# Performance work log

Measured on AMD Instinct MI355X. Metric: run time of the kernel, lower is better.

## Reference

```python
import jax, jax.numpy as jnp
import numpy as np


def _maxpool(x, k):
    # non-overlapping kxk max pool (kernel == stride), NCHW
    B, C, H, W = x.shape
    return x.reshape(B, C, H // k, k, W // k, k).max(axis=(3, 5))


def setup_inputs() -> dict:
    key = jax.random.key(0)
    k1, k2, k3, k4 = jax.random.split(key, 4)
    return {
        "x1": jax.random.normal(k1, (8, 128, 128, 128), dtype=jnp.float32),
        "x2": jax.random.normal(k2, (8, 32, 256, 256), dtype=jnp.float32),
        "x3": jax.random.normal(k3, (8, 2, 512, 512), dtype=jnp.float32),
        "pure_ff": jax.random.normal(k4, (8, 256, 64, 64), dtype=jnp.float32),
    }


def reference(x1, x2, x3, pure_ff):
    # torch.cat([x,x],1) repeated n times duplicates the whole channel block
    # 2^n times; pooling duplicated channels equals pooling once then tiling.
    y1 = jnp.tile(_maxpool(x1, 2), (1, 2, 1, 1))    # 1 cat  -> x2 channels
    y2 = jnp.tile(_maxpool(x2, 4), (1, 8, 1, 1))    # 3 cats -> x8 channels
    y3 = jnp.tile(_maxpool(x3, 8), (1, 128, 1, 1))  # 7 cats -> x128 channels
    return jax.nn.relu(y1 + y2 + y3 + pure_ff)
```

## Files before the change

kernel.cpp:

```cpp
#include <hip/hip_runtime.h>
#include <math.h>


__global__ __launch_bounds__(256) void fused_ff_block3(
    const float* __restrict__ x1, const float* __restrict__ x2,
    const float* __restrict__ x3, const float* __restrict__ ff,
    float* __restrict__ out)
{
    __shared__ float y2s[32][64];
    __shared__ float y3s[2][64];

    const int bid = blockIdx.x;
    const int b   = bid >> 6;
    const int h   = bid & 63;
    const int tid = threadIdx.x;

    if (tid < 128) {
        const int c3 = tid >> 6;
        const int w  = tid & 63;
        const float* p = x3 + (size_t)b * 524288 + (size_t)c3 * 262144
                            + (size_t)(h * 8) * 512 + (size_t)w * 8;
        float m = -INFINITY;
        #pragma unroll
        for (int r = 0; r < 8; ++r) {
            const float4 a = *reinterpret_cast<const float4*>(p + (size_t)r * 512);
            const float4 c = *reinterpret_cast<const float4*>(p + (size_t)r * 512 + 4);
            m = fmaxf(m, fmaxf(fmaxf(fmaxf(a.x, a.y), fmaxf(a.z, a.w)),
                               fmaxf(fmaxf(c.x, c.y), fmaxf(c.z, c.w))));
        }
        y3s[c3][w] = m;
    }

    #pragma unroll
    for (int v = tid; v < 2048; v += 256) {
        const int c2 = v >> 6;
        const int w  = v & 63;
        const float* p = x2 + (size_t)b * 2097152 + (size_t)c2 * 65536
                            + (size_t)(h * 4) * 256 + (size_t)w * 4;
        float m = -INFINITY;
        #pragma unroll
        for (int r = 0; r < 4; ++r) {
            const float4 a = *reinterpret_cast<const float4*>(p + (size_t)r * 256);
            m = fmaxf(m, fmaxf(fmaxf(a.x, a.y), fmaxf(a.z, a.w)));
        }
        y2s[c2][w] = m;
    }

    __syncthreads();

    const int w     = tid & 63;
    const int clane = tid >> 6;
    #pragma unroll 4
    for (int it = 0; it < 32; ++it) {
        const int c1 = it * 4 + clane;
        const float* p = x1 + (size_t)b * 2097152 + (size_t)c1 * 16384
                            + (size_t)(h * 2) * 128 + (size_t)w * 2;
        const float2 a  = *reinterpret_cast<const float2*>(p);
        const float2 bb = *reinterpret_cast<const float2*>(p + 128);
        const float p1 = fmaxf(fmaxf(a.x, a.y), fmaxf(bb.x, bb.y));
        const float s  = p1 + y2s[c1 & 31][w] + y3s[c1 & 1][w];

        const size_t obase = (size_t)b * 1048576 + (size_t)h * 64 + (size_t)w;
        const size_t o0 = obase + (size_t)c1 * 4096;
        const size_t o1 = obase + (size_t)(c1 + 128) * 4096;
        out[o0] = fmaxf(s + ff[o0], 0.0f);
        out[o1] = fmaxf(s + ff[o1], 0.0f);
    }
}

extern "C" void kernel_launch(void* const* d_in, const int* in_sizes, int n_in,
                              void* d_out, int out_size, void* d_ws, size_t ws_size,
                              hipStream_t stream) {
    const float* x1 = (const float*)d_in[0];
    const float* x2 = (const float*)d_in[1];
    const float* x3 = (const float*)d_in[2];
    const float* ff = (const float*)d_in[3];
    float* out = (float*)d_out;

    dim3 grid(512);
    dim3 block(256);
    fused_ff_block3<<<grid, block, 0, stream>>>(x1, x2, x3, ff, out);
}
```

Measured before the change: 37.06 us.

## Split rows into width quarters, vectorize loads/stores, shuffle-reduce x3 pooling

```diff
diff --git a/kernel.cpp b/kernel.cpp
--- a/kernel.cpp
+++ b/kernel.cpp
@@ -2,69 +2,101 @@
 #include <math.h>
 
 
-__global__ __launch_bounds__(256) void fused_ff_block3(
+__global__ __launch_bounds__(256, 8) void fused_ff_block3(
     const float* __restrict__ x1, const float* __restrict__ x2,
     const float* __restrict__ x3, const float* __restrict__ ff,
     float* __restrict__ out)
 {
-    __shared__ float y2s[32][64];
-    __shared__ float y3s[2][64];
+    __shared__ float y2s[32][16];
+    __shared__ float y3s[2][16];
 
     const int bid = blockIdx.x;
-    const int b   = bid >> 6;
-    const int h   = bid & 63;
+    const int wq  = bid & 3;
+    const int h   = (bid >> 2) & 63;
+    const int b   = bid >> 8;
     const int tid = threadIdx.x;
 
-    if (tid < 128) {
-        const int c3 = tid >> 6;
-        const int w  = tid & 63;
-        const float* p = x3 + (size_t)b * 524288 + (size_t)c3 * 262144
-                            + (size_t)(h * 8) * 512 + (size_t)w * 8;
-        float m = -INFINITY;
-        #pragma unroll
-        for (int r = 0; r < 8; ++r) {
-            const float4 a = *reinterpret_cast<const float4*>(p + (size_t)r * 512);
-            const float4 c = *reinterpret_cast<const float4*>(p + (size_t)r * 512 + 4);
-            m = fmaxf(m, fmaxf(fmaxf(fmaxf(a.x, a.y), fmaxf(a.z, a.w)),
-                               fmaxf(fmaxf(c.x, c.y), fmaxf(c.z, c.w))));
-        }
-        y3s[c3][w] = m;
+    const int lane = tid & 63;
+    const int o3   = (tid >> 6) * 8 + (lane >> 3);
+    const int r3   = lane & 7;
+    const int c3   = o3 >> 4;
+    const int w3   = o3 & 15;
+    const float* p3 = x3 + (size_t)b * 524288 + (size_t)c3 * 262144
+                    + (size_t)(h * 8 + r3) * 512 + (size_t)(wq * 16 + w3) * 8;
+    const float4 a3 = *reinterpret_cast<const float4*>(p3);
+    const float4 b3 = *reinterpret_cast<const float4*>(p3 + 4);
+
+    #pragma unroll
+    for (int it = 0; it < 2; ++it) {
+        const int v  = tid + it * 256;
+        const int c2 = v >> 4;
+        const int w2 = v & 15;
+        const float* p = x2 + (size_t)b * 2097152 + (size_t)c2 * 65536
+                       + (size_t)(h * 4) * 256 + (size_t)(wq * 16 + w2) * 4;
+        const float4 q0 = *reinterpret_cast<const float4*>(p);
+        const float4 q1 = *reinterpret_cast<const float4*>(p + 256);
+        const float4 q2 = *reinterpret_cast<const float4*>(p + 512);
+        const float4 q3 = *reinterpret_cast<const float4*>(p + 768);
+        float m = fmaxf(fmaxf(fmaxf(q0.x, q0.y), fmaxf(q0.z, q0.w)),
+                        fmaxf(fmaxf(q1.x, q1.y), fmaxf(q1.z, q1.w)));
+        m = fmaxf(m, fmaxf(fmaxf(q2.x, q2.y), fmaxf(q2.z, q2.w)));
+        m = fmaxf(m, fmaxf(fmaxf(q3.x, q3.y), fmaxf(q3.z, q3.w)));
+        y2s[c2][w2] = m;
     }
 
-    #pragma unroll
-    for (int v = tid; v < 2048; v += 256) {
-        const int c2 = v >> 6;
-        const int w  = v & 63;
-        const float* p = x2 + (size_t)b * 2097152 + (size_t)c2 * 65536
-                            + (size_t)(h * 4) * 256 + (size_t)w * 4;
-        float m = -INFINITY;
-        #pragma unroll
-        for (int r = 0; r < 4; ++r) {
-            const float4 a = *reinterpret_cast<const float4*>(p + (size_t)r * 256);
-            m = fmaxf(m, fmaxf(fmaxf(a.x, a.y), fmaxf(a.z, a.w)));
-        }
-        y2s[c2][w] = m;
-    }
+    float m3 = fmaxf(fmaxf(fmaxf(a3.x, a3.y), fmaxf(a3.z, a3.w)),
+                     fmaxf(fmaxf(b3.x, b3.y), fmaxf(b3.z, b3.w)));
+    m3 = fmaxf(m3, __shfl_xor(m3, 1, 64));
+    m3 = fmaxf(m3, __shfl_xor(m3, 2, 64));
+    m3 = fmaxf(m3, __shfl_xor(m3, 4, 64));
+    if (r3 == 0) y3s[c3][w3] = m3;
 
     __syncthreads();
 
-    const int w     = tid & 63;
-    const int clane = tid >> 6;
-    #pragma unroll 4
-    for (int it = 0; it < 32; ++it) {
-        const int c1 = it * 4 + clane;
+    const int w4  = tid & 3;
+    const int c1b = tid >> 2;
+    #pragma unroll
+    for (int it = 0; it < 2; ++it) {
+        const int c1 = c1b + it * 64;
         const float* p = x1 + (size_t)b * 2097152 + (size_t)c1 * 16384
-                            + (size_t)(h * 2) * 128 + (size_t)w * 2;
-        const float2 a  = *reinterpret_cast<const float2*>(p);
-        const float2 bb = *reinterpret_cast<const float2*>(p + 128);
-        const float p1 = fmaxf(fmaxf(a.x, a.y), fmaxf(bb.x, bb.y));
-        const float s  = p1 + y2s[c1 & 31][w] + y3s[c1 & 1][w];
+                       + (size_t)(h * 2) * 128 + (size_t)(wq * 16 + w4 * 4) * 2;
+        const float4 a0 = *reinterpret_cast<const float4*>(p);
+        const float4 a1 = *reinterpret_cast<const float4*>(p + 4);
+        const float4 r0 = *reinterpret_cast<const float4*>(p + 128);
+        const float4 r1 = *reinterpret_cast<const float4*>(p + 132);
+        float4 y1v;
+        y1v.x = fmaxf(fmaxf(a0.x, a0.y), fmaxf(r0.x, r0.y));
+        y1v.y = fmaxf(fmaxf(a0.z, a0.w), fmaxf(r0.z, r0.w));
+        y1v.z = fmaxf(fmaxf(a1.x, a1.y), fmaxf(r1.x, r1.y));
+        y1v.w = fmaxf(fmaxf(a1.z, a1.w), fmaxf(r1.z, r1.w));
 
-        const size_t obase = (size_t)b * 1048576 + (size_t)h * 64 + (size_t)w;
-        const size_t o0 = obase + (size_t)c1 * 4096;
-        const size_t o1 = obase + (size_t)(c1 + 128) * 4096;
-        out[o0] = fmaxf(s + ff[o0], 0.0f);
-        out[o1] = fmaxf(s + ff[o1], 0.0f);
+        const float4 y2v = *reinterpret_cast<const float4*>(&y2s[c1 & 31][w4 * 4]);
+        const float4 y3v = *reinterpret_cast<const float4*>(&y3s[c1 & 1][w4 * 4]);
+
+        const size_t o0 = (size_t)b * 1048576 + (size_t)c1 * 4096
+                        + (size_t)h * 64 + (size_t)(wq * 16 + w4 * 4);
+        const size_t o1 = o0 + (size_t)128 * 4096;
+        const float4 f0 = *reinterpret_cast<const float4*>(ff + o0);
+        const float4 f1 = *reinterpret_cast<const float4*>(ff + o1);
+
+        float4 s;
+        s.x = y1v.x + y2v.x + y3v.x;
+        s.y = y1v.y + y2v.y + y3v.y;
+        s.z = y1v.z + y2v.z + y3v.z;
+        s.w = y1v.w + y2v.w + y3v.w;
+
+        float4 u0, u1;
+        u0.x = fmaxf(s.x + f0.x, 0.0f);
+        u0.y = fmaxf(s.y + f0.y, 0.0f);
+        u0.z = fmaxf(s.z + f0.z, 0.0f);
+        u0.w = fmaxf(s.w + f0.w, 0.0f);
+        u1.x = fmaxf(s.x + f1.x, 0.0f);
+        u1.y = fmaxf(s.y + f1.y, 0.0f);
+        u1.z = fmaxf(s.z + f1.z, 0.0f);
+        u1.w = fmaxf(s.w + f1.w, 0.0f);
+
+        *reinterpret_cast<float4*>(out + o0) = u0;
+        *reinterpret_cast<float4*>(out + o1) = u1;
     }
 }
 
@@ -77,7 +109,7 @@
     const float* ff = (const float*)d_in[3];
     float* out = (float*)d_out;
 
-    dim3 grid(512);
+    dim3 grid(2048);
     dim3 block(256);
     fused_ff_block3<<<grid, block, 0, stream>>>(x1, x2, x3, ff, out);
 }
```

After: 41.57 us. +12.2%, slower.

## Split into pooling and combine kernels using workspace intermediates

Applied to the files above, without the earlier changes.

```diff
diff --git a/kernel.cpp b/kernel.cpp
--- a/kernel.cpp
+++ b/kernel.cpp
@@ -1,6 +1,104 @@
 #include <hip/hip_runtime.h>
 #include <math.h>
 
+
+__global__ __launch_bounds__(256) void pool_kernel(
+    const float* __restrict__ x2, const float* __restrict__ x3,
+    float* __restrict__ y2, float* __restrict__ y3)
+{
+    const int bid = blockIdx.x;
+    if (bid < 4096) {
+        const int t = bid * 256 + threadIdx.x;
+        const int w = t & 63;
+        const int h = (t >> 6) & 63;
+        const int c = (t >> 12) & 31;
+        const int b = t >> 17;
+        const float* p = x2 + (size_t)b * 2097152 + (size_t)c * 65536
+                            + (size_t)(h * 4) * 256 + (size_t)w * 4;
+        float m = -INFINITY;
+        #pragma unroll
+        for (int r = 0; r < 4; ++r) {
+            const float4 a = *reinterpret_cast<const float4*>(p + (size_t)r * 256);
+            m = fmaxf(m, fmaxf(fmaxf(a.x, a.y), fmaxf(a.z, a.w)));
+        }
+        y2[t] = m;
+    } else {
+        const int t = (bid - 4096) * 256 + threadIdx.x;
+        const int w = t & 63;
+        const int h = (t >> 6) & 63;
+        const int c = (t >> 12) & 1;
+        const int b = t >> 13;
+        const float* p = x3 + (size_t)b * 524288 + (size_t)c * 262144
+                            + (size_t)(h * 8) * 512 + (size_t)w * 8;
+        float m = -INFINITY;
+        #pragma unroll
+        for (int r = 0; r < 8; ++r) {
+            const float4 a  = *reinterpret_cast<const float4*>(p + (size_t)r * 512);
+            const float4 c4 = *reinterpret_cast<const float4*>(p + (size_t)r * 512 + 4);
+            m = fmaxf(m, fmaxf(fmaxf(fmaxf(a.x, a.y), fmaxf(a.z, a.w)),
+                               fmaxf(fmaxf(c4.x, c4.y), fmaxf(c4.z, c4.w))));
+        }
+        y3[t] = m;
+    }
+}
+
+__global__ __launch_bounds__(256) void combine_kernel(
+    const float* __restrict__ x1, const float* __restrict__ ff,
+    const float* __restrict__ y2, const float* __restrict__ y3,
+    float* __restrict__ out)
+{
+    const int bid = blockIdx.x;
+    const int b   = bid >> 7;
+    const int c   = bid & 127;
+
+    const size_t x1_base = (size_t)b * 2097152 + (size_t)c * 16384;
+    const size_t o0_base = (size_t)b * 1048576 + (size_t)c * 4096;
+    const size_t o1_base = o0_base + (size_t)128 * 4096;
+    const size_t y2_base = (size_t)b * 131072 + (size_t)(c & 31) * 4096;
+    const size_t y3_base = (size_t)b * 8192   + (size_t)(c & 1)  * 4096;
+
+    #pragma unroll
+    for (int it = 0; it < 4; ++it) {
+        const int f  = it * 256 + threadIdx.x;
+        const int w4 = f & 15;
+        const int h  = f >> 4;
+
+        const float* p = x1 + x1_base + (size_t)(2 * h) * 128 + (size_t)w4 * 8;
+        const float4 a0 = *reinterpret_cast<const float4*>(p);
+        const float4 a1 = *reinterpret_cast<const float4*>(p + 4);
+        const float4 r0 = *reinterpret_cast<const float4*>(p + 128);
+        const float4 r1 = *reinterpret_cast<const float4*>(p + 132);
+        float4 y1v;
+        y1v.x = fmaxf(fmaxf(a0.x, a0.y), fmaxf(r0.x, r0.y));
+        y1v.y = fmaxf(fmaxf(a0.z, a0.w), fmaxf(r0.z, r0.w));
+        y1v.z = fmaxf(fmaxf(a1.x, a1.y), fmaxf(r1.x, r1.y));
+        y1v.w = fmaxf(fmaxf(a1.z, a1.w), fmaxf(r1.z, r1.w));
+
+        const float4 y2v = *reinterpret_cast<const float4*>(y2 + y2_base + (size_t)f * 4);
+        const float4 y3v = *reinterpret_cast<const float4*>(y3 + y3_base + (size_t)f * 4);
+        const float4 f0  = *reinterpret_cast<const float4*>(ff + o0_base + (size_t)f * 4);
+        const float4 f1  = *reinterpret_cast<const float4*>(ff + o1_base + (size_t)f * 4);
+
+        float4 s;
+        s.x = y1v.x + y2v.x + y3v.x;
+        s.y = y1v.y + y2v.y + y3v.y;
+        s.z = y1v.z + y2v.z + y3v.z;
+        s.w = y1v.w + y2v.w + y3v.w;
+
+        float4 u0, u1;
+        u0.x = fmaxf(s.x + f0.x, 0.0f);
+        u0.y = fmaxf(s.y + f0.y, 0.0f);
+        u0.z = fmaxf(s.z + f0.z, 0.0f);
+        u0.w = fmaxf(s.w + f0.w, 0.0f);
+        u1.x = fmaxf(s.x + f1.x, 0.0f);
+        u1.y = fmaxf(s.y + f1.y, 0.0f);
+        u1.z = fmaxf(s.z + f1.z, 0.0f);
+        u1.w = fmaxf(s.w + f1.w, 0.0f);
+
+        *reinterpret_cast<float4*>(out + o0_base + (size_t)f * 4) = u0;
+        *reinterpret_cast<float4*>(out + o1_base + (size_t)f * 4) = u1;
+    }
+}
 
 __global__ __launch_bounds__(256) void fused_ff_block3(
     const float* __restrict__ x1, const float* __restrict__ x2,
@@ -30,7 +128,6 @@
         }
         y3s[c3][w] = m;
     }
-
     #pragma unroll
     for (int v = tid; v < 2048; v += 256) {
         const int c2 = v >> 6;
@@ -45,9 +142,7 @@
         }
         y2s[c2][w] = m;
     }
-
     __syncthreads();
-
     const int w     = tid & 63;
     const int clane = tid >> 6;
     #pragma unroll 4
@@ -59,7 +154,6 @@
         const float2 bb = *reinterpret_cast<const float2*>(p + 128);
         const float p1 = fmaxf(fmaxf(a.x, a.y), fmaxf(bb.x, bb.y));
         const float s  = p1 + y2s[c1 & 31][w] + y3s[c1 & 1][w];
-
         const size_t obase = (size_t)b * 1048576 + (size_t)h * 64 + (size_t)w;
         const size_t o0 = obase + (size_t)c1 * 4096;
         const size_t o1 = obase + (size_t)(c1 + 128) * 4096;
@@ -77,7 +171,13 @@
     const float* ff = (const float*)d_in[3];
     float* out = (float*)d_out;
 
-    dim3 grid(512);
-    dim3 block(256);
-    fused_ff_block3<<<grid, block, 0, stream>>>(x1, x2, x3, ff, out);
+    const size_t need = (size_t)(1048576 + 65536) * sizeof(float);
+    if (ws_size >= need) {
+        float* y2 = (float*)d_ws;
+        float* y3 = y2 + 1048576;
+        pool_kernel<<<dim3(4352), dim3(256), 0, stream>>>(x2, x3, y2, y3);
+        combine_kernel<<<dim3(1024), dim3(256), 0, stream>>>(x1, ff, y2, y3, out);
+    } else {
+        fused_ff_block3<<<dim3(512), dim3(256), 0, stream>>>(x1, x2, x3, ff, out);
+    }
 }
```

After: 38.82 us. 1.05x slower.
